# Kernel tuning notes

Measured on AMD Instinct MI355X. Metric: run time of the kernel, lower is better.

The kernel has to match this reference:

```python
import jax, jax.numpy as jnp
import numpy as np
from jax import lax

KSIZE = 7
EPS = 1e-10


def _circular_mask(k=KSIZE):
    # faithful to EdgeLoss.cal_mask: inclusive circle, normalized by count
    xs = np.arange(k, dtype=np.float32)
    d2 = (xs[:, None] + 0.5 - k / 2) ** 2 + (xs[None, :] + 0.5 - k / 2) ** 2
    m = (d2 <= ((k - 1) / 2) ** 2).astype(np.float32)
    return jnp.asarray(m / m.sum())


def _gather_logp(prob, target):
    # prob: (B,C,H,W), target: (B,H,W) int -> log prob at target class, (B,1,H,W)
    logpt = jnp.log(prob + EPS)
    return jnp.take_along_axis(logpt, target[:, None, :, :], axis=1)


def _focal0(prob, target):
    # FocalLoss(gamma=0, alpha=None): mean of -log p_t
    return jnp.mean(-_gather_logp(prob, target))


def _dice(prob, target):
    t = target.astype(prob.dtype)          # (B,H,W)
    p = prob[:, 1, :, :]                   # foreground channel
    I = jnp.sum(p * t, axis=(1, 2))
    U = jnp.sum(p + t, axis=(1, 2))
    return 1.0 - jnp.mean(2.0 * I / (U + EPS))


def _edge(prob, target, mask):
    # circular box-filter average of target == unfold+mask sum (zero padding)
    t = target.astype(prob.dtype)[:, None, :, :]  # (B,1,H,W)
    ave = lax.conv_general_dilated(t, mask[None, None, :, :], (1, 1), 'SAME')
    at = jnp.abs(t - ave)                          # edge weight (B,1,H,W)
    lp = _gather_logp(prob, target)                # (B,1,H,W)
    return jnp.mean(-lp * at)


def _calloss(prob, target, sigmas, mask):
    return (_focal0(prob, target) / sigmas[0]
            + _dice(prob, target) / sigmas[1]
            + _edge(prob, target, mask) / sigmas[2])


def setup_inputs() -> dict:
    key = jax.random.key(0)
    k1, k2, k3, k4, k5 = jax.random.split(key, 5)
    N, M, B, C, H, W = 2, 1, 8, 2, 1024, 1024
    predictions = jax.random.normal(k1, (N, B, C, H, W), dtype=jnp.float32)
    Diss = jax.random.uniform(k2, (M, B, C, H, W), dtype=jnp.float32)
    target = jax.random.randint(k3, (B, H, W), 0, 2, dtype=jnp.int32)
    diff = jax.random.normal(k4, (), dtype=jnp.float32)
    sigma = jax.random.uniform(k5, (3,), dtype=jnp.float32, minval=0.5, maxval=1.5)
    return {"predictions": predictions, "Diss": Diss, "target": target,
            "diff": diff, "sigma": sigma}


def reference(predictions, Diss, target, diff, sigma):
    mask = _circular_mask()
    sigmas = sigma * sigma
    loss = jnp.asarray(0.0, dtype=predictions.dtype)
    for i in range(predictions.shape[0]):            # deep-supervision heads
        prob = jax.nn.softmax(predictions[i], axis=1)
        loss = loss + _calloss(prob, target, sigmas, mask)
    for j in range(Diss.shape[0]):                   # already-probabilities
        loss = loss + _calloss(Diss[j], target, sigmas, mask)
    loss = loss + diff                               # len(diff) != 0 branch
    loss = loss + jnp.sum(jnp.log(sigmas)) / 2
    return loss
```

## Files before the change

kernel.cpp:

```cpp
#include <hip/hip_runtime.h>
#include <math.h>

#define BB 8
#define HH 1024
#define WW 1024
#define HW (1024*1024)

#define TW 128
#define TH 16
#define HALO_H (TH+6)
#define TSTRIDE 136
#define NCOPY 32
#define NSLOT 18

__global__ __launch_bounds__(256)
void loss_main(const float* __restrict__ pred,
               const float* __restrict__ diss,
               const int*   __restrict__ target,
               double*      __restrict__ acc)
{
    __shared__ float tile[HALO_H][TSTRIDE];
    __shared__ float h5[HALO_H][TW];
    __shared__ float h7[HALO_H][TW];
    __shared__ float red[4][12];

    const int bx = blockIdx.x;
    const int by = blockIdx.y;
    const int b  = blockIdx.z;
    const int x0 = bx * TW, y0 = by * TH;
    const int tid = threadIdx.x;
    const int txx = tid & 31;
    const int ty  = tid >> 5;

    const int* tgt_b = target + (size_t)b * HW;
    for (int ch = tid; ch < HALO_H * 34; ch += 256) {
        int r = ch / 34;
        int m = ch - r * 34;
        int gy  = y0 - 3 + r;
        int gxb = x0 - 4 + 4 * m;
        float4 v = make_float4(0.f, 0.f, 0.f, 0.f);
        if (gy >= 0 && gy < HH) {
            if (gxb >= 0 && gxb + 3 < WW) {
                const int4 iv = *(const int4*)(tgt_b + (size_t)gy * WW + gxb);
                v.x = (float)iv.x; v.y = (float)iv.y;
                v.z = (float)iv.z; v.w = (float)iv.w;
            } else {
                #pragma unroll
                for (int j = 0; j < 4; ++j) {
                    int gx = gxb + j;
                    ((float*)&v)[j] = (gx >= 0 && gx < WW)
                        ? (float)tgt_b[(size_t)gy * WW + gx] : 0.f;
                }
            }
        }
        *(float4*)&tile[r][4 * m] = v;
    }
    __syncthreads();

    for (int g = tid; g < HALO_H * 32; g += 256) {
        int r  = g >> 5;
        int xg = (g & 31) << 2;
        float4 c0 = *(const float4*)&tile[r][xg];
        float4 c1 = *(const float4*)&tile[r][xg + 4];
        float4 c2 = *(const float4*)&tile[r][xg + 8];
        float s1 = c0.y, s2 = c0.z, s3 = c0.w;
        float s4 = c1.x, s5 = c1.y, s6 = c1.z, s7 = c1.w;
        float s8 = c2.x, s9 = c2.y, s10 = c2.z;
        float4 v5, v7;
        v5.x = s2 + s3 + s4 + s5 + s6;
        v5.y = s3 + s4 + s5 + s6 + s7;
        v5.z = s4 + s5 + s6 + s7 + s8;
        v5.w = s5 + s6 + s7 + s8 + s9;
        v7.x = v5.x + s1 + s7;
        v7.y = v5.y + s2 + s8;
        v7.z = v5.z + s3 + s9;
        v7.w = v5.w + s4 + s10;
        *(float4*)&h5[r][xg] = v5;
        *(float4*)&h7[r][xg] = v7;
    }
    __syncthreads();

    const float* p00 = pred + ((size_t)(0 * BB + b) * 2 + 0) * HW;
    const float* p01 = p00 + HW;
    const float* p10 = pred + ((size_t)(1 * BB + b) * 2 + 0) * HW;
    const float* p11 = p10 + HW;
    const float* q0  = diss + ((size_t)b * 2 + 0) * HW;
    const float* q1  = q0 + HW;

    float sf0=0.f, se0=0.f, si0=0.f, su0=0.f;
    float sf1=0.f, se1=0.f, si1=0.f, su1=0.f;
    float sf2=0.f, se2=0.f, si2=0.f, su2=0.f;

    const int x  = txx * 4;
    const int gx = x0 + x;
    #pragma unroll
    for (int k = 0; k < 2; ++k) {
        const int r  = ty + 8 * k;
        const int gy = y0 + r;
        const size_t off = (size_t)gy * WW + gx;

        float4 t4  = *(const float4*)&tile[r + 3][x + 4];
        float4 top = *(const float4*)&tile[r    ][x + 4];
        float4 bot = *(const float4*)&tile[r + 6][x + 4];
        float4 a1v = *(const float4*)&h5[r + 1][x];
        float4 a2v = *(const float4*)&h5[r + 2][x];
        float4 a3v = *(const float4*)&h7[r + 3][x];
        float4 a4v = *(const float4*)&h5[r + 4][x];
        float4 a5v = *(const float4*)&h5[r + 5][x];

        float4 v00 = *(const float4*)(p00 + off);
        float4 v01 = *(const float4*)(p01 + off);
        float4 v10 = *(const float4*)(p10 + off);
        float4 v11 = *(const float4*)(p11 + off);
        float4 w0  = *(const float4*)(q0  + off);
        float4 w1  = *(const float4*)(q1  + off);

        float4 cnt;
        cnt.x = top.x + a1v.x + a2v.x + a3v.x + a4v.x + a5v.x + bot.x;
        cnt.y = top.y + a1v.y + a2v.y + a3v.y + a4v.y + a5v.y + bot.y;
        cnt.z = top.z + a1v.z + a2v.z + a3v.z + a4v.z + a5v.z + bot.z;
        cnt.w = top.w + a1v.w + a2v.w + a3v.w + a4v.w + a5v.w + bot.w;

        #pragma unroll
        for (int j = 0; j < 4; ++j) {
            const float t  = ((const float*)&t4)[j];
            const float at = fabsf(t - ((const float*)&cnt)[j] * (1.0f / 29.0f));
            {
                float a0 = ((const float*)&v00)[j], a1 = ((const float*)&v01)[j];
                float p1v = __builtin_amdgcn_rcpf(1.0f + __expf(a0 - a1));
                float pt  = (t != 0.0f) ? p1v : 1.0f - p1v;
                float lp  = __logf(pt + 1e-10f);
                sf0 -= lp; se0 -= lp * at; si0 += p1v * t; su0 += p1v + t;
            }
            {
                float a0 = ((const float*)&v10)[j], a1 = ((const float*)&v11)[j];
                float p1v = __builtin_amdgcn_rcpf(1.0f + __expf(a0 - a1));
                float pt  = (t != 0.0f) ? p1v : 1.0f - p1v;
                float lp  = __logf(pt + 1e-10f);
                sf1 -= lp; se1 -= lp * at; si1 += p1v * t; su1 += p1v + t;
            }
            {
                float d0 = ((const float*)&w0)[j], d1 = ((const float*)&w1)[j];
                float pt = (t != 0.0f) ? d1 : d0;
                float lp = __logf(pt + 1e-10f);
                sf2 -= lp; se2 -= lp * at; si2 += d1 * t; su2 += d1 + t;
            }
        }
    }

    float vals[12] = {sf0,se0,si0,su0, sf1,se1,si1,su1, sf2,se2,si2,su2};
    #pragma unroll
    for (int j = 0; j < 12; ++j) {
        float v = vals[j];
        #pragma unroll
        for (int s = 32; s > 0; s >>= 1) v += __shfl_down(v, s, 64);
        vals[j] = v;
    }
    const int wave = tid >> 6;
    const int lane = tid & 63;
    if (lane == 0) {
        #pragma unroll
        for (int j = 0; j < 12; ++j) red[wave][j] = vals[j];
    }
    __syncthreads();
    if (tid < 12) {
        double s = (double)red[0][tid] + (double)red[1][tid]
                 + (double)red[2][tid] + (double)red[3][tid];
        const int img  = tid >> 2;
        const int what = tid & 3;
        int slot;
        if      (what == 0) slot = 0;
        else if (what == 1) slot = 1;
        else if (what == 2) slot = 2 + b;
        else                slot = 10 + b;
        const int copy = (by * 8 + bx) & (NCOPY - 1);
        unsafeAtomicAdd(acc + ((size_t)(img * NSLOT + slot) * NCOPY + copy), s);
    }
}

__global__ __launch_bounds__(256)
void finalize_kernel(const double* __restrict__ acc,
                     const float*  __restrict__ diff,
                     const float*  __restrict__ sigma,
                     float*        __restrict__ out)
{
    __shared__ double ssum[54];
    const int t = threadIdx.x;
    if (t < 216) {
        const int slot_lin = t >> 2;
        const int part     = t & 3;
        const double* p = acc + (size_t)slot_lin * NCOPY + part * 8;
        double s = 0.0;
        #pragma unroll
        for (int j = 0; j < 8; ++j) s += p[j];
        s += __shfl_down(s, 1, 64);
        s += __shfl_down(s, 2, 64);
        if (part == 0) ssum[slot_lin] = s;
    }
    __syncthreads();
    if (t == 0) {
        const double sig0 = (double)sigma[0] * (double)sigma[0];
        const double sig1 = (double)sigma[1] * (double)sigma[1];
        const double sig2 = (double)sigma[2] * (double)sigma[2];
        const double inv  = 1.0 / (double)((size_t)BB * HW);
        double loss = 0.0;
        for (int i = 0; i < 3; ++i) {
            const double* A = ssum + i * NSLOT;
            double focal = A[0] * inv;
            double edge  = A[1] * inv;
            double dsum  = 0.0;
            for (int b = 0; b < BB; ++b)
                dsum += 2.0 * A[2 + b] / (A[10 + b] + 1e-10);
            double dice = 1.0 - dsum / (double)BB;
            loss += focal / sig0 + dice / sig1 + edge / sig2;
        }
        loss += (double)diff[0];
        loss += 0.5 * (log(sig0) + log(sig1) + log(sig2));
        out[0] = (float)loss;
    }
}

extern "C" void kernel_launch(void* const* d_in, const int* in_sizes, int n_in,
                              void* d_out, int out_size, void* d_ws, size_t ws_size,
                              hipStream_t stream)
{
    const float* pred   = (const float*)d_in[0];
    const float* diss   = (const float*)d_in[1];
    const int*   target = (const int*)  d_in[2];
    const float* diff   = (const float*)d_in[3];
    const float* sigma  = (const float*)d_in[4];
    double* acc = (double*)d_ws;

    hipMemsetAsync(d_ws, 0, (size_t)3 * NSLOT * NCOPY * sizeof(double), stream);

    dim3 grid(WW / TW, HH / TH, BB);
    loss_main<<<grid, 256, 0, stream>>>(pred, diss, target, acc);
    finalize_kernel<<<1, 256, 0, stream>>>(acc, diff, sigma, (float*)d_out);
}
```

Measured before the change: 268.2 us.

## Pack target halo into bytes and fuse finalize via last-block reduction

Stores the target tile and the horizontal box sums as packed 8-bit values in shared memory, so the vertical sum becomes SWAR integer adds instead of float4 adds. This cuts LDS footprint and LDS traffic. The separate finalize kernel is folded into the main kernel with an atomic counter, and the last block to finish does the final reduction, saving one launch. It also requests higher occupancy through launch bounds. Risks are byte overflow, which stays safe because the count is at most 29, and the threadfence/atomic ordering cost.

After: 463.5 us. 1.73x slower.

```diff
diff --git a/kernel.cpp b/kernel.cpp
--- a/kernel.cpp
+++ b/kernel.cpp
@@ -12,17 +12,23 @@
 #define TSTRIDE 136
 #define NCOPY 32
 #define NSLOT 18
-
-__global__ __launch_bounds__(256)
+#define NBLOCKS (8*64*8)
+
+__global__ __launch_bounds__(256, 8)
 void loss_main(const float* __restrict__ pred,
                const float* __restrict__ diss,
                const int*   __restrict__ target,
-               double*      __restrict__ acc)
+               double*      __restrict__ acc,
+               const float* __restrict__ diff,
+               const float* __restrict__ sigma,
+               float*       __restrict__ out)
 {
-    __shared__ float tile[HALO_H][TSTRIDE];
-    __shared__ float h5[HALO_H][TW];
-    __shared__ float h7[HALO_H][TW];
+    __shared__ unsigned char tileb[HALO_H][TSTRIDE];
+    __shared__ unsigned char h5b[HALO_H][TW];
+    __shared__ unsigned char h7b[HALO_H][TW];
     __shared__ float red[4][12];
+    __shared__ double ssum[54];
+    __shared__ int lastflag;
 
     const int bx = blockIdx.x;
     const int by = blockIdx.y;
@@ -38,45 +44,47 @@
         int m = ch - r * 34;
         int gy  = y0 - 3 + r;
         int gxb = x0 - 4 + 4 * m;
-        float4 v = make_float4(0.f, 0.f, 0.f, 0.f);
+        unsigned pk = 0u;
         if (gy >= 0 && gy < HH) {
             if (gxb >= 0 && gxb + 3 < WW) {
                 const int4 iv = *(const int4*)(tgt_b + (size_t)gy * WW + gxb);
-                v.x = (float)iv.x; v.y = (float)iv.y;
-                v.z = (float)iv.z; v.w = (float)iv.w;
+                pk = (unsigned)iv.x | ((unsigned)iv.y << 8)
+                   | ((unsigned)iv.z << 16) | ((unsigned)iv.w << 24);
             } else {
                 #pragma unroll
                 for (int j = 0; j < 4; ++j) {
                     int gx = gxb + j;
-                    ((float*)&v)[j] = (gx >= 0 && gx < WW)
-                        ? (float)tgt_b[(size_t)gy * WW + gx] : 0.f;
+                    if (gx >= 0 && gx < WW)
+                        pk |= ((unsigned)tgt_b[(size_t)gy * WW + gx]) << (8 * j);
                 }
             }
         }
-        *(float4*)&tile[r][4 * m] = v;
+        *(unsigned*)&tileb[r][4 * m] = pk;
     }
     __syncthreads();
 
     for (int g = tid; g < HALO_H * 32; g += 256) {
         int r  = g >> 5;
         int xg = (g & 31) << 2;
-        float4 c0 = *(const float4*)&tile[r][xg];
-        float4 c1 = *(const float4*)&tile[r][xg + 4];
-        float4 c2 = *(const float4*)&tile[r][xg + 8];
-        float s1 = c0.y, s2 = c0.z, s3 = c0.w;
-        float s4 = c1.x, s5 = c1.y, s6 = c1.z, s7 = c1.w;
-        float s8 = c2.x, s9 = c2.y, s10 = c2.z;
-        float4 v5, v7;
-        v5.x = s2 + s3 + s4 + s5 + s6;
-        v5.y = s3 + s4 + s5 + s6 + s7;
-        v5.z = s4 + s5 + s6 + s7 + s8;
-        v5.w = s5 + s6 + s7 + s8 + s9;
-        v7.x = v5.x + s1 + s7;
-        v7.y = v5.y + s2 + s8;
-        v7.z = v5.z + s3 + s9;
-        v7.w = v5.w + s4 + s10;
-        *(float4*)&h5[r][xg] = v5;
-        *(float4*)&h7[r][xg] = v7;
+        const unsigned char* row = &tileb[r][0];
+        unsigned d0 = *(const unsigned*)(row + xg);
+        unsigned d1 = *(const unsigned*)(row + xg + 4);
+        unsigned d2 = *(const unsigned*)(row + xg + 8);
+        int s1 = (d0 >> 8) & 255, s2 = (d0 >> 16) & 255, s3 = (d0 >> 24) & 255;
+        int s4 = d1 & 255, s5 = (d1 >> 8) & 255, s6 = (d1 >> 16) & 255, s7 = (d1 >> 24) & 255;
+        int s8 = d2 & 255, s9 = (d2 >> 8) & 255, s10 = (d2 >> 16) & 255;
+        int v5x = s2 + s3 + s4 + s5 + s6;
+        int v5y = v5x - s2 + s7;
+        int v5z = v5y - s3 + s8;
+        int v5w = v5z - s4 + s9;
+        int v7x = v5x + s1 + s7;
+        int v7y = v5y + s2 + s8;
+        int v7z = v5z + s3 + s9;
+        int v7w = v5w + s4 + s10;
+        *(unsigned*)&h5b[r][xg] = (unsigned)v5x | ((unsigned)v5y << 8)
+                                | ((unsigned)v5z << 16) | ((unsigned)v5w << 24);
+        *(unsigned*)&h7b[r][xg] = (unsigned)v7x | ((unsigned)v7y << 8)
+                                | ((unsigned)v7z << 16) | ((unsigned)v7w << 24);
     }
     __syncthreads();
 
@@ -99,51 +107,48 @@
         const int gy = y0 + r;
         const size_t off = (size_t)gy * WW + gx;
 
-        float4 t4  = *(const float4*)&tile[r + 3][x + 4];
-        float4 top = *(const float4*)&tile[r    ][x + 4];
-        float4 bot = *(const float4*)&tile[r + 6][x + 4];
-        float4 a1v = *(const float4*)&h5[r + 1][x];
-        float4 a2v = *(const float4*)&h5[r + 2][x];
-        float4 a3v = *(const float4*)&h7[r + 3][x];
-        float4 a4v = *(const float4*)&h5[r + 4][x];
-        float4 a5v = *(const float4*)&h5[r + 5][x];
-
-        float4 v00 = *(const float4*)(p00 + off);
-        float4 v01 = *(const float4*)(p01 + off);
-        float4 v10 = *(const float4*)(p10 + off);
-        float4 v11 = *(const float4*)(p11 + off);
-        float4 w0  = *(const float4*)(q0  + off);
-        float4 w1  = *(const float4*)(q1  + off);
-
-        float4 cnt;
-        cnt.x = top.x + a1v.x + a2v.x + a3v.x + a4v.x + a5v.x + bot.x;
-        cnt.y = top.y + a1v.y + a2v.y + a3v.y + a4v.y + a5v.y + bot.y;
-        cnt.z = top.z + a1v.z + a2v.z + a3v.z + a4v.z + a5v.z + bot.z;
-        cnt.w = top.w + a1v.w + a2v.w + a3v.w + a4v.w + a5v.w + bot.w;
+        const unsigned tq  = *(const unsigned*)&tileb[r + 3][x + 4];
+        const unsigned top = *(const unsigned*)&tileb[r    ][x + 4];
+        const unsigned bot = *(const unsigned*)&tileb[r + 6][x + 4];
+        const unsigned c1  = *(const unsigned*)&h5b[r + 1][x];
+        const unsigned c2  = *(const unsigned*)&h5b[r + 2][x];
+        const unsigned c3  = *(const unsigned*)&h7b[r + 3][x];
+        const unsigned c4  = *(const unsigned*)&h5b[r + 4][x];
+        const unsigned c5  = *(const unsigned*)&h5b[r + 5][x];
+        const unsigned cnt = top + bot + c1 + c2 + c3 + c4 + c5;
+
+        const float4 v00 = *(const float4*)(p00 + off);
+        const float4 v01 = *(const float4*)(p01 + off);
+        const float4 v10 = *(const float4*)(p10 + off);
+        const float4 v11 = *(const float4*)(p11 + off);
+        const float4 w0  = *(const float4*)(q0  + off);
+        const float4 w1  = *(const float4*)(q1  + off);
 
         #pragma unroll
         for (int j = 0; j < 4; ++j) {
-            const float t  = ((const float*)&t4)[j];
-            const float at = fabsf(t - ((const float*)&cnt)[j] * (1.0f / 29.0f));
+            const unsigned tbit = (tq >> (8 * j)) & 1u;
+            const float tf = (float)tbit;
+            const float cj = (float)((cnt >> (8 * j)) & 0xffu);
+            const float at = fabsf(tf - cj * (1.0f / 29.0f));
             {
                 float a0 = ((const float*)&v00)[j], a1 = ((const float*)&v01)[j];
                 float p1v = __builtin_amdgcn_rcpf(1.0f + __expf(a0 - a1));
-                float pt  = (t != 0.0f) ? p1v : 1.0f - p1v;
+                float pt  = tbit ? p1v : 1.0f - p1v;
                 float lp  = __logf(pt + 1e-10f);
-                sf0 -= lp; se0 -= lp * at; si0 += p1v * t; su0 += p1v + t;
+                sf0 -= lp; se0 -= lp * at; si0 += p1v * tf; su0 += p1v + tf;
             }
             {
                 float a0 = ((const float*)&v10)[j], a1 = ((const float*)&v11)[j];
                 float p1v = __builtin_amdgcn_rcpf(1.0f + __expf(a0 - a1));
-                float pt  = (t != 0.0f) ? p1v : 1.0f - p1v;
+                float pt  = tbit ? p1v : 1.0f - p1v;
                 float lp  = __logf(pt + 1e-10f);
-                sf1 -= lp; se1 -= lp * at; si1 += p1v * t; su1 += p1v + t;
+                sf1 -= lp; se1 -= lp * at; si1 += p1v * tf; su1 += p1v + tf;
             }
             {
                 float d0 = ((const float*)&w0)[j], d1 = ((const float*)&w1)[j];
-                float pt = (t != 0.0f) ? d1 : d0;
+                float pt = tbit ? d1 : d0;
                 float lp = __logf(pt + 1e-10f);
-                sf2 -= lp; se2 -= lp * at; si2 += d1 * t; su2 += d1 + t;
+                sf2 -= lp; se2 -= lp * at; si2 += d1 * tf; su2 += d1 + tf;
             }
         }
     }
@@ -176,47 +181,49 @@
         const int copy = (by * 8 + bx) & (NCOPY - 1);
         unsafeAtomicAdd(acc + ((size_t)(img * NSLOT + slot) * NCOPY + copy), s);
     }
-}
-
-__global__ __launch_bounds__(256)
-void finalize_kernel(const double* __restrict__ acc,
-                     const float*  __restrict__ diff,
-                     const float*  __restrict__ sigma,
-                     float*        __restrict__ out)
-{
-    __shared__ double ssum[54];
-    const int t = threadIdx.x;
-    if (t < 216) {
-        const int slot_lin = t >> 2;
-        const int part     = t & 3;
-        const double* p = acc + (size_t)slot_lin * NCOPY + part * 8;
-        double s = 0.0;
-        #pragma unroll
-        for (int j = 0; j < 8; ++j) s += p[j];
-        s += __shfl_down(s, 1, 64);
-        s += __shfl_down(s, 2, 64);
-        if (part == 0) ssum[slot_lin] = s;
-    }
-    __syncthreads();
-    if (t == 0) {
-        const double sig0 = (double)sigma[0] * (double)sigma[0];
-        const double sig1 = (double)sigma[1] * (double)sigma[1];
-        const double sig2 = (double)sigma[2] * (double)sigma[2];
-        const double inv  = 1.0 / (double)((size_t)BB * HW);
-        double loss = 0.0;
-        for (int i = 0; i < 3; ++i) {
-            const double* A = ssum + i * NSLOT;
-            double focal = A[0] * inv;
-            double edge  = A[1] * inv;
-            double dsum  = 0.0;
-            for (int b = 0; b < BB; ++b)
-                dsum += 2.0 * A[2 + b] / (A[10 + b] + 1e-10);
-            double dice = 1.0 - dsum / (double)BB;
-            loss += focal / sig0 + dice / sig1 + edge / sig2;
-        }
-        loss += (double)diff[0];
-        loss += 0.5 * (log(sig0) + log(sig1) + log(sig2));
-        out[0] = (float)loss;
+    __syncthreads();
+
+    unsigned* counter = (unsigned*)(acc + 54 * NCOPY);
+    if (tid == 0) {
+        __threadfence();
+        unsigned old = atomicAdd(counter, 1u);
+        lastflag = (old == NBLOCKS - 1) ? 1 : 0;
+    }
+    __syncthreads();
+    if (lastflag) {
+        __threadfence();
+        if (tid < 216) {
+            const int sl = tid >> 2, part = tid & 3;
+            const double* p = acc + (size_t)sl * NCOPY + part * 8;
+            double s = 0.0;
+            #pragma unroll
+            for (int j = 0; j < 8; ++j)
+                s += __hip_atomic_load(&p[j], __ATOMIC_RELAXED, __HIP_MEMORY_SCOPE_AGENT);
+            s += __shfl_down(s, 1, 64);
+            s += __shfl_down(s, 2, 64);
+            if (part == 0) ssum[sl] = s;
+        }
+        __syncthreads();
+        if (tid == 0) {
+            const double sig0 = (double)sigma[0] * (double)sigma[0];
+            const double sig1 = (double)sigma[1] * (double)sigma[1];
+            const double sig2 = (double)sigma[2] * (double)sigma[2];
+            const double inv  = 1.0 / (double)((size_t)BB * HW);
+            double loss = 0.0;
+            for (int i = 0; i < 3; ++i) {
+                const double* A = ssum + i * NSLOT;
+                double focal = A[0] * inv;
+                double edge  = A[1] * inv;
+                double dsum  = 0.0;
+                for (int bb = 0; bb < BB; ++bb)
+                    dsum += 2.0 * A[2 + bb] / (A[10 + bb] + 1e-10);
+                double dice = 1.0 - dsum / (double)BB;
+                loss += focal / sig0 + dice / sig1 + edge / sig2;
+            }
+            loss += (double)diff[0];
+            loss += 0.5 * (log(sig0) + log(sig1) + log(sig2));
+            out[0] = (float)loss;
+        }
     }
 }
 
@@ -231,9 +238,9 @@
     const float* sigma  = (const float*)d_in[4];
     double* acc = (double*)d_ws;
 
-    hipMemsetAsync(d_ws, 0, (size_t)3 * NSLOT * NCOPY * sizeof(double), stream);
+    hipMemsetAsync(d_ws, 0, (size_t)54 * NCOPY * sizeof(double) + 16, stream);
 
     dim3 grid(WW / TW, HH / TH, BB);
-    loss_main<<<grid, 256, 0, stream>>>(pred, diss, target, acc);
-    finalize_kernel<<<1, 256, 0, stream>>>(acc, diff, sigma, (float*)d_out);
+    loss_main<<<grid, 256, 0, stream>>>(pred, diss, target, acc, diff, sigma,
+                                        (float*)d_out);
 }
```
